# Kernel tuning notes

Hardware: AMD Instinct MI355X
Metric: run time of the kernel (lower is better)

## Reference

```python
import jax, jax.numpy as jnp
import numpy as np
from jax import lax

B, T, H, W, C = 2, 32, 65, 65, 32
KS = 15   # kernel_size
F = 32    # conv features


def setup_inputs() -> dict:
    key = jax.random.key(0)
    ks = jax.random.split(key, 12)
    d = {}
    d["input_seq"] = jax.random.normal(ks[0], (B, T, H, W, C), jnp.float32)
    d["conv_w"] = jax.random.normal(ks[1], (3, 3, C, F), jnp.float32) / np.sqrt(3 * 3 * C).astype(np.float32)
    d["conv_b"] = jnp.zeros((F,), jnp.float32)
    for i, nm in enumerate(["alpha", "delta", "mu", "gamma"]):
        d[f"w_{nm}"] = jax.random.normal(ks[2 + i], (F, C), jnp.float32) / np.sqrt(F).astype(np.float32)
        d[f"b_{nm}"] = jnp.zeros((C,), jnp.float32)
    # nn.initializers.normal() -> stddev 0.01
    d["k_exc"] = jax.random.normal(ks[10], (KS, KS, C), jnp.float32) * 0.01
    d["k_inh"] = jax.random.normal(ks[11], (KS, KS, C), jnp.float32) * 0.01
    return d


def _kernel_spec(k, Hh, Ww):
    # zero-pad the (KS,KS,C) kernel to (H,W,C), then rfft2 over spatial axes
    ph, pw = (Hh - KS) // 2, (Ww - KS) // 2
    kp = jnp.pad(k, ((ph, ph), (pw, pw), (0, 0)))
    return jnp.fft.rfft2(kp, axes=(0, 1))  # (H, W//2+1, C) complex64


def reference(input_seq, conv_w, conv_b, w_alpha, b_alpha, w_delta, b_delta,
              w_mu, b_mu, w_gamma, b_gamma, k_exc, k_inh):
    Bb, Tt, Hh, Ww, Cc = input_seq.shape
    # context conv: flax Conv flattens leading (B,T) into batch; SAME, stride 2
    x = input_seq.reshape(Bb * Tt, Hh, Ww, Cc)
    stats = lax.conv_general_dilated(x, conv_w, (2, 2), 'SAME',
                                     dimension_numbers=('NHWC', 'HWIO', 'NHWC')) + conv_b
    stats = jax.nn.gelu(stats)  # flax nn.gelu (approximate)
    Hp, Wp = stats.shape[1], stats.shape[2]
    stats = stats.reshape(Bb, Tt, Hp, Wp, F)
    ctx = jnp.mean(stats, axis=(1, 2))                 # (B, Wp, F); Wp == W//2+1 for odd W
    alpha = jax.nn.sigmoid(ctx @ w_alpha + b_alpha)    # (B, Wp, C)
    delta = jax.nn.sigmoid(ctx @ w_delta + b_delta)
    mu = jax.nn.softplus(ctx @ w_mu + b_mu)
    gamma = jax.nn.softplus(ctx @ w_gamma + b_gamma)

    K_E = _kernel_spec(k_exc, Hh, Ww)  # (H, Wr, C)
    K_I = _kernel_spec(k_inh, Hh, Ww)
    Wr = Ww // 2 + 1
    decay = jnp.asarray(0.9, jnp.complex64)

    bc = lambda v: jnp.broadcast_to(v[:, None, :, :].astype(jnp.complex64), (Bb, Hh, Wr, Cc))
    A_xx = decay * bc(alpha)
    A_yy = decay * bc(delta)
    A_xy = -K_I[None] * bc(mu)
    A_yx = K_E[None] * bc(gamma)
    row0 = jnp.stack([A_xx, A_xy], axis=-1)
    row1 = jnp.stack([A_yx, A_yy], axis=-1)
    K_hat = jnp.stack([row0, row1], axis=-2)           # (B, H, Wr, C, 2, 2)

    U_hat = jnp.fft.rfft2(input_seq, axes=(2, 3))      # (B, T, H, Wr, C) complex64
    U_vec = jnp.stack([U_hat, jnp.zeros_like(U_hat)], axis=-1)  # (B,T,H,Wr,C,2)
    A_t = jnp.broadcast_to(K_hat[:, None], (Bb, Tt, Hh, Wr, Cc, 2, 2))

    # associative op for linear SSM: state_t = A_t @ state_{t-1} + u_t
    # (log/exp of the original cancel: exp(log A)=A, exp(State_log)=State)
    def combine(l, r):
        A1, b1 = l
        A2, b2 = r
        A = jnp.einsum('...ij,...jk->...ik', A2, A1)
        b = jnp.einsum('...ij,...j->...i', A2, b1) + b2
        return A, b

    _, S = lax.associative_scan(combine, (A_t, U_vec), axis=1)
    Y = S[..., 1]                                      # inhibitory component
    return jnp.fft.irfft2(Y, axes=(2, 3))              # (B, T, H, 2*(Wr-1), C) float32
```

## Files before the change

### kernel.cpp

```cpp
#include <hip/hip_runtime.h>
#include <cmath>

#define NB 2
#define NT 32
#define NH 65
#define NW 65
#define NC 32
#define NF 32
#define NKS 15
#define NHP 33
#define NWP 33
#define NWR 33
#define NWOUT 64
#define PI_F 3.14159265358979323846f

using bf16x8 = __attribute__((ext_vector_type(8))) __bf16;
using f32x4  = __attribute__((ext_vector_type(4))) float;
using s16x4  = __attribute__((ext_vector_type(4))) short;

__device__ inline unsigned short f2bf(float v) {
    unsigned u = __float_as_uint(v);
    u = u + 0x7FFF + ((u >> 16) & 1);
    return (unsigned short)(u >> 16);
}
__device__ inline float bf2f(unsigned short h) {
    return __uint_as_float((unsigned)h << 16);
}

union FragU { s16x4 h[2]; bf16x8 v; };

__global__ __launch_bounds__(256) void setup_kernel(
    const float* __restrict__ w, unsigned short* __restrict__ wBh,
    unsigned short* __restrict__ wBl,
    float2* __restrict__ twr, float2* __restrict__ twb, float2* __restrict__ twi)
{
    int blk = blockIdx.x;
    if (blk < 10) {
        int tid = blk * 256 + threadIdx.x;
        if (tid < NH * 36) {
            int q = tid / 36, wr = tid % 36;
            float2 v = make_float2(0.f, 0.f);
            if (wr < NWR) {
                int p = (q * wr) % NH;
                float a = -2.f * PI_F * (float)p / (float)NH;
                v = make_float2(cosf(a), sinf(a));
            }
            twr[tid] = v;
        }
        if (tid < NH * 14) {
            int h = tid / 14, b = tid % 14;
            float2 v = make_float2(0.f, 0.f);
            if (b < 13) {
                int p = (h * b) % NH;
                float a = 2.f * PI_F * (float)p / (float)NH;
                v = make_float2(cosf(a), sinf(a));
            }
            twb[tid] = v;
        }
        if (tid < 31 * 64) {
            int q = tid / 64 + 1, ow = tid % 64;
            int p = (q * ow) & 63;
            float a = 2.f * PI_F * (float)p / (float)NWOUT;
            twi[tid] = make_float2(cosf(a), sinf(a));
        }
    } else {
        int tid = (blk - 10) * 256 + threadIdx.x;
        if (tid < 9 * NF * NC) {
            int dd = tid / 1024;
            int f = (tid / 32) % 32;
            int c = tid % 32;
            float v = w[((size_t)dd * NC + c) * NF + f];
            unsigned short h = f2bf(v);
            wBh[tid] = h;
            wBl[tid] = f2bf(v - bf2f(h));
        }
    }
}

__global__ __launch_bounds__(256) void conv_mfma_kernel(
    const float* __restrict__ x, const unsigned short* __restrict__ wBh,
    const unsigned short* __restrict__ wBl, const float* __restrict__ bias,
    float* __restrict__ partial)
{
    __shared__ unsigned short aH[3 * 68 * 36];
    __shared__ unsigned short aL[3 * 68 * 36];
    int blk = blockIdx.x;
    int i = blk % NHP;
    int bt = blk / NHP;
    int tid = threadIdx.x;
    int l = tid & 63;
    int w = tid >> 6;

    int nt = w & 1;
    int fcol = nt * 16 + (l & 15);
    int c0 = (l >> 4) * 8;
    bf16x8 bh[9], bl[9];
    #pragma unroll
    for (int dd = 0; dd < 9; ++dd) {
        bh[dd] = *(const bf16x8*)(wBh + dd * 1024 + fcol * 32 + c0);
        bl[dd] = *(const bf16x8*)(wBl + dd * 1024 + fcol * 32 + c0);
    }

    const float* xb = x + (size_t)bt * (NH * NW * NC);
    for (int q = tid; q < 3 * 68 * 8; q += 256) {
        int r = q / 544;
        int k = q % 544;
        int pcol = k >> 3;
        int c4 = (k & 7) * 4;
        int gr = 2 * i - 1 + r;
        int gcol = pcol - 1;
        float4 v = make_float4(0.f, 0.f, 0.f, 0.f);
        if (gr >= 0 && gr < NH && gcol >= 0 && gcol < NW)
            v = *(const float4*)(xb + ((size_t)gr * NW + gcol) * NC + c4);
        int base = (r * 68 + pcol) * 36 + c4;
        unsigned short h0 = f2bf(v.x), h1 = f2bf(v.y), h2 = f2bf(v.z), h3 = f2bf(v.w);
        s16x4 th = {(short)h0, (short)h1, (short)h2, (short)h3};
        *(s16x4*)(aH + base) = th;
        s16x4 tl = {(short)f2bf(v.x - bf2f(h0)), (short)f2bf(v.y - bf2f(h1)),
                    (short)f2bf(v.z - bf2f(h2)), (short)f2bf(v.w - bf2f(h3))};
        *(s16x4*)(aL + base) = tl;
    }
    __syncthreads();

    float bv = bias[fcol];
    f32x4 acc0 = {bv, bv, bv, bv};
    f32x4 acc1 = {bv, bv, bv, bv};
    const int mtA = (w >> 1) ? 1 : 0;
    const bool hasB = (w >> 1) == 0;
    int m15 = l & 15;

    #pragma unroll
    for (int dd = 0; dd < 9; ++dd) {
        const int di = dd / 3, dj = dd % 3;
        {
            int pcol = 2 * (mtA * 16 + m15) + dj;
            int off = (di * 68 + pcol) * 36 + c0;
            FragU ah, al;
            ah.h[0] = *(const s16x4*)(aH + off);
            ah.h[1] = *(const s16x4*)(aH + off + 4);
            al.h[0] = *(const s16x4*)(aL + off);
            al.h[1] = *(const s16x4*)(aL + off + 4);
            acc0 = __builtin_amdgcn_mfma_f32_16x16x32_bf16(al.v, bh[dd], acc0, 0, 0, 0);
            acc0 = __builtin_amdgcn_mfma_f32_16x16x32_bf16(ah.v, bl[dd], acc0, 0, 0, 0);
            acc0 = __builtin_amdgcn_mfma_f32_16x16x32_bf16(ah.v, bh[dd], acc0, 0, 0, 0);
        }
        if (hasB) {
            int pcol = 2 * (32 + m15) + dj;
            if (pcol > 67) pcol = 67;
            int off = (di * 68 + pcol) * 36 + c0;
            FragU ah, al;
            ah.h[0] = *(const s16x4*)(aH + off);
            ah.h[1] = *(const s16x4*)(aH + off + 4);
            al.h[0] = *(const s16x4*)(aL + off);
            al.h[1] = *(const s16x4*)(aL + off + 4);
            acc1 = __builtin_amdgcn_mfma_f32_16x16x32_bf16(al.v, bh[dd], acc1, 0, 0, 0);
            acc1 = __builtin_amdgcn_mfma_f32_16x16x32_bf16(ah.v, bl[dd], acc1, 0, 0, 0);
            acc1 = __builtin_amdgcn_mfma_f32_16x16x32_bf16(ah.v, bh[dd], acc1, 0, 0, 0);
        }
    }

    float* pout = partial + (size_t)blk * (NWP * NF);
    int g4 = (l >> 4) * 4;
    #define GELU(v) (0.5f * (v) * (1.f + tanhf(0.7978845608028654f * ((v) + 0.044715f * (v) * (v) * (v)))))
    #pragma unroll
    for (int r = 0; r < 4; ++r) {
        float v = acc0[r];
        pout[(mtA * 16 + g4 + r) * NF + fcol] = GELU(v);
    }
    if (hasB && g4 == 0) {
        float v = acc1[0];
        pout[32 * NF + fcol] = GELU(v);
    }
    #undef GELU
}

__global__ __launch_bounds__(256) void ctx_reduce1_kernel(
    const float* __restrict__ partial, float* __restrict__ red2)
{
    __shared__ float red[4][64];
    int blk = blockIdx.x;
    int b = blk / 136;
    int rem = blk % 136;
    int chunk = rem / 8;
    int ts = rem % 8;
    int lane = threadIdx.x & 63;
    int tig = threadIdx.x >> 6;
    int jf = chunk * 64 + lane;
    float s0 = 0.f, s1 = 0.f, s2 = 0.f;
    if (jf < NWP * NF) {
        const float* p = partial + (size_t)b * (NT * NHP) * (NWP * NF)
                       + (size_t)(ts * 132 + tig * 33) * (NWP * NF) + jf;
        #pragma unroll 3
        for (int s = 0; s < 33; s += 3) {
            s0 += p[(size_t)s * (NWP * NF)];
            s1 += p[(size_t)(s + 1) * (NWP * NF)];
            s2 += p[(size_t)(s + 2) * (NWP * NF)];
        }
    }
    red[tig][lane] = s0 + s1 + s2;
    __syncthreads();
    if (threadIdx.x < 64) {
        float tot = red[0][threadIdx.x] + red[1][threadIdx.x] +
                    red[2][threadIdx.x] + red[3][threadIdx.x];
        red2[((b * 17 + chunk) * 8 + ts) * 64 + threadIdx.x] = tot;
    }
}

__global__ __launch_bounds__(256) void ctx_reduce2_kernel(
    const float* __restrict__ red2, float* __restrict__ ctx)
{
    __shared__ float red[4][64];
    int b = blockIdx.x / 17, chunk = blockIdx.x % 17;
    int lane = threadIdx.x & 63, tg = threadIdx.x >> 6;
    const float* r2 = red2 + ((size_t)(b * 17 + chunk) * 8) * 64;
    float v = r2[(2 * tg) * 64 + lane] + r2[(2 * tg + 1) * 64 + lane];
    red[tg][lane] = v;
    __syncthreads();
    if (threadIdx.x < 64) {
        int jf = chunk * 64 + threadIdx.x;
        if (jf < NWP * NF) {
            float tot = red[0][threadIdx.x] + red[1][threadIdx.x] +
                        red[2][threadIdx.x] + red[3][threadIdx.x];
            ctx[b * (NWP * NF) + jf] = tot * (1.f / (NT * NHP));
        }
    }
}

__global__ __launch_bounds__(256) void gate_kernel(
    const float* __restrict__ ctx,
    const float* __restrict__ wA, const float* __restrict__ bA,
    const float* __restrict__ wD, const float* __restrict__ bD,
    const float* __restrict__ wM, const float* __restrict__ bM,
    const float* __restrict__ wG, const float* __restrict__ bG,
    float* __restrict__ alpha, float* __restrict__ delta,
    float* __restrict__ mu, float* __restrict__ gamma)
{
    int idx = blockIdx.x * 256 + threadIdx.x;
    if (idx >= NB * NWP * NC) return;
    int c = idx % NC;
    int bw = idx / NC;
    float sA = bA[c], sD = bD[c], sM = bM[c], sG = bG[c];
    #pragma unroll
    for (int f = 0; f < NF; ++f) {
        float v = ctx[bw * NF + f];
        sA = fmaf(v, wA[f * NC + c], sA);
        sD = fmaf(v, wD[f * NC + c], sD);
        sM = fmaf(v, wM[f * NC + c], sM);
        sG = fmaf(v, wG[f * NC + c], sG);
    }
    alpha[idx] = 1.f / (1.f + expf(-sA));
    delta[idx] = 1.f / (1.f + expf(-sD));
    mu[idx]    = fmaxf(sM, 0.f) + log1pf(expf(-fabsf(sM)));
    gamma[idx] = fmaxf(sG, 0.f) + log1pf(expf(-fabsf(sG)));
}

__global__ __launch_bounds__(256) void spec_kernel(
    const float* __restrict__ kexc, const float* __restrict__ kinh,
    float2* __restrict__ KE, float2* __restrict__ KI)
{
    __shared__ float2 tw[NH];
    int tid = threadIdx.x;
    if (tid < NH) {
        float a = -2.f * PI_F * (float)tid / (float)NH;
        tw[tid] = make_float2(cosf(a), sinf(a));
    }
    __syncthreads();
    int idx = blockIdx.x * 256 + tid;
    if (idx >= NH * NWR * NC) return;
    int c = idx % NC;
    int rem = idx / NC;
    int wr = rem % NWR;
    int h = rem / NWR;
    float ker = 0, kei = 0, kir = 0, kii = 0;
    int prow = (25 * (h + wr)) % NH;
    for (int i = 0; i < NKS; ++i) {
        int p = prow;
        for (int j = 0; j < NKS; ++j) {
            float2 e = tw[p];
            float ve = kexc[(i * NKS + j) * NC + c];
            float vi = kinh[(i * NKS + j) * NC + c];
            ker = fmaf(ve, e.x, ker); kei = fmaf(ve, e.y, kei);
            kir = fmaf(vi, e.x, kir); kii = fmaf(vi, e.y, kii);
            p += wr; if (p >= NH) p -= NH;
        }
        prow += h; if (prow >= NH) prow -= NH;
    }
    KE[idx] = make_float2(ker, kei);
    KI[idx] = make_float2(kir, kii);
}

__global__ __launch_bounds__(256) void dft_rows_kernel(
    const float* __restrict__ x, const float2* __restrict__ twr_g,
    float2* __restrict__ U1)
{
    __shared__ __align__(16) float row[4][NW * NC];
    __shared__ __align__(16) float2 twt[NH * 36];
    int tid = threadIdx.x;
    int blk = blockIdx.x;
    int grp = blk % 17;
    int bt = blk / 17;
    int hbase = grp * 4;
    int nrows = NH - hbase; if (nrows > 4) nrows = 4;

    const float* xp = x + ((size_t)bt * NH + hbase) * (NW * NC);
    for (int idx = tid; idx < nrows * NW * NC; idx += 256) ((float*)row)[idx] = xp[idx];
    for (int idx = tid; idx < NH * 36; idx += 256) twt[idx] = twr_g[idx];
    __syncthreads();

    int c = tid & 31;
    int jg = tid >> 5;
    float2 acc[4][4];
    #pragma unroll
    for (int r = 0; r < 4; ++r)
        #pragma unroll
        for (int k = 0; k < 4; ++k) acc[r][k] = make_float2(0.f, 0.f);

    const float2* tp = twt + 4 * jg;
    #pragma unroll 5
    for (int q = 0; q < NW; ++q) {
        float4 e01 = *(const float4*)&tp[q * 36];
        float4 e23 = *(const float4*)&tp[q * 36 + 2];
        #pragma unroll
        for (int r = 0; r < 4; ++r) {
            float v = row[r][q * NC + c];
            acc[r][0].x = fmaf(v, e01.x, acc[r][0].x); acc[r][0].y = fmaf(v, e01.y, acc[r][0].y);
            acc[r][1].x = fmaf(v, e01.z, acc[r][1].x); acc[r][1].y = fmaf(v, e01.w, acc[r][1].y);
            acc[r][2].x = fmaf(v, e23.x, acc[r][2].x); acc[r][2].y = fmaf(v, e23.y, acc[r][2].y);
            acc[r][3].x = fmaf(v, e23.z, acc[r][3].x); acc[r][3].y = fmaf(v, e23.w, acc[r][3].y);
        }
    }
    #pragma unroll
    for (int r = 0; r < 4; ++r) {
        if (r < nrows) {
            float2* up = U1 + ((size_t)bt * NH + hbase + r) * (NWR * NC);
            up[(4 * jg + 0) * NC + c] = acc[r][0];
            up[(4 * jg + 1) * NC + c] = acc[r][1];
            up[(4 * jg + 2) * NC + c] = acc[r][2];
            up[(4 * jg + 3) * NC + c] = acc[r][3];
        }
    }
    if (jg == 0) {
        float2 a32[4];
        #pragma unroll
        for (int r = 0; r < 4; ++r) a32[r] = make_float2(0.f, 0.f);
        #pragma unroll 5
        for (int q = 0; q < NW; ++q) {
            float2 e = twt[q * 36 + 32];
            #pragma unroll
            for (int r = 0; r < 4; ++r) {
                float v = row[r][q * NC + c];
                a32[r].x = fmaf(v, e.x, a32[r].x);
                a32[r].y = fmaf(v, e.y, a32[r].y);
            }
        }
        #pragma unroll
        for (int r = 0; r < 4; ++r)
            if (r < nrows)
                U1[((size_t)bt * NH + hbase + r) * (NWR * NC) + 32 * NC + c] = a32[r];
    }
}

template <int SIGN>
__device__ inline void compute5(const float2 v[5], float2* outp) {
    const float C5[5] = {1.f, 0.30901699437494742f, -0.80901699437494745f,
                         -0.80901699437494745f, 0.30901699437494742f};
    const float S5[5] = {0.f, 0.95105651629515357f, 0.58778525229247314f,
                         -0.58778525229247314f, -0.95105651629515357f};
    #pragma unroll
    for (int r = 0; r < 5; ++r) {
        float re = 0.f, im = 0.f;
        #pragma unroll
        for (int a = 0; a < 5; ++a) {
            const int m = (r * a) % 5;
            const float ex = C5[m];
            const float ey = (float)SIGN * S5[m];
            re = fmaf(v[a].x, ex, fmaf(-v[a].y, ey, re));
            im = fmaf(v[a].x, ey, fmaf(v[a].y, ex, im));
        }
        outp[r * NC] = make_float2(re, im);
    }
}

template <int SIGN, bool SCALE>
__global__ __launch_bounds__(256) void dft_cols_kernel(
    const float2* __restrict__ in, float2* __restrict__ out,
    const float2* __restrict__ twb_g)
{
    __shared__ __align__(16) float2 col[NH * NC];
    __shared__ __align__(16) float2 twb[NH * 14];
    int tid = threadIdx.x;
    int blk = blockIdx.x;
    int wr = blk % NWR;
    int bt = blk / NWR;
    const float2* ip = in + ((size_t)bt * NH) * (NWR * NC) + wr * NC;
    for (int idx = tid; idx < NH * NC; idx += 256) {
        int p = idx >> 5, c = idx & 31;
        col[idx] = ip[(size_t)p * (NWR * NC) + c];
    }
    for (int idx = tid; idx < NH * 14; idx += 256) twb[idx] = twb_g[idx];
    __syncthreads();

    float2 va0[5], va1[5];
    int bq0 = tid >> 5, c0 = tid & 31;
    int q1 = tid + 256;
    int bq1 = q1 >> 5, c1 = q1 & 31;
    #pragma unroll
    for (int a = 0; a < 5; ++a) {
        va0[a] = col[(13 * a + bq0) * NC + c0];
        if (q1 < 416) va1[a] = col[(13 * a + bq1) * NC + c1];
    }
    __syncthreads();
    compute5<SIGN>(va0, &col[(bq0 * 5) * NC + c0]);
    if (q1 < 416) compute5<SIGN>(va1, &col[(bq1 * 5) * NC + c1]);
    __syncthreads();

    const float S = (float)SIGN;
    int c = tid & 31;
    int h0 = tid >> 5;
    const float s = SCALE ? (1.f / (float)NH) : 1.f;
    float2* op = out + ((size_t)bt * NH) * (NWR * NC) + wr * NC;
    float2 acc[8];
    #pragma unroll
    for (int k = 0; k < 8; ++k) {
        int h = h0 + 8 * k;
        int r = h % 5;
        const float2* Ap = col + r * NC + c;
        const float2* tp = twb + h * 14;
        float re = 0.f, im = 0.f;
        #pragma unroll
        for (int p = 0; p < 6; ++p) {
            float4 tq = *(const float4*)&tp[2 * p];
            float2 v0 = Ap[(2 * p) * 5 * NC];
            float2 v1 = Ap[(2 * p + 1) * 5 * NC];
            re = fmaf(v0.x, tq.x, fmaf(-S * v0.y, tq.y, re));
            im = fmaf(S * v0.x, tq.y, fmaf(v0.y, tq.x, im));
            re = fmaf(v1.x, tq.z, fmaf(-S * v1.y, tq.w, re));
            im = fmaf(S * v1.x, tq.w, fmaf(v1.y, tq.z, im));
        }
        {
            float2 t12 = tp[12];
            float2 v = Ap[12 * 5 * NC];
            re = fmaf(v.x, t12.x, fmaf(-S * v.y, t12.y, re));
            im = fmaf(S * v.x, t12.y, fmaf(v.y, t12.x, im));
        }
        acc[k] = make_float2(re * s, im * s);
    }
    #pragma unroll
    for (int k = 0; k < 8; ++k) {
        int h = h0 + 8 * k;
        op[(size_t)h * (NWR * NC) + c] = acc[k];
    }
    if (h0 == 0) {
        const float2* Ap = col + 4 * NC + c;
        const float2* tp = twb + 64 * 14;
        float re = 0.f, im = 0.f;
        #pragma unroll
        for (int p = 0; p < 6; ++p) {
            float4 tq = *(const float4*)&tp[2 * p];
            float2 v0 = Ap[(2 * p) * 5 * NC];
            float2 v1 = Ap[(2 * p + 1) * 5 * NC];
            re = fmaf(v0.x, tq.x, fmaf(-S * v0.y, tq.y, re));
            im = fmaf(S * v0.x, tq.y, fmaf(v0.y, tq.x, im));
            re = fmaf(v1.x, tq.z, fmaf(-S * v1.y, tq.w, re));
            im = fmaf(S * v1.x, tq.w, fmaf(v1.y, tq.z, im));
        }
        {
            float2 t12 = tp[12];
            float2 v = Ap[12 * 5 * NC];
            re = fmaf(v.x, t12.x, fmaf(-S * v.y, t12.y, re));
            im = fmaf(S * v.x, t12.y, fmaf(v.y, t12.x, im));
        }
        op[(size_t)64 * (NWR * NC) + c] = make_float2(re * s, im * s);
    }
}

__global__ __launch_bounds__(256) void scan_kernel(
    float2* __restrict__ buf, const float2* __restrict__ KE,
    const float2* __restrict__ KI, const float* __restrict__ alpha,
    const float* __restrict__ delta, const float* __restrict__ mu,
    const float* __restrict__ gamma)
{
    int idx = blockIdx.x * 256 + threadIdx.x;
    if (idx >= NB * NH * NWR * NC) return;
    int c = idx % NC;
    int rem = idx / NC;
    int wr = rem % NWR;
    int rem2 = rem / NWR;
    int h = rem2 % NH;
    int b = rem2 / NH;

    int gi = (b * NWP + wr) * NC + c;
    float axx = 0.9f * alpha[gi];
    float ayy = 0.9f * delta[gi];
    float m = mu[gi], g = gamma[gi];
    float2 ki = KI[(h * NWR + wr) * NC + c];
    float2 ke = KE[(h * NWR + wr) * NC + c];
    float2 axy = make_float2(-ki.x * m, -ki.y * m);
    float2 ayx = make_float2(ke.x * g, ke.y * g);

    float2 xs = make_float2(0.f, 0.f), ys = make_float2(0.f, 0.f);
    size_t base = ((size_t)b * NT) * NH * NWR * NC + (size_t)h * (NWR * NC) + wr * NC + c;
    const size_t stride = (size_t)NH * NWR * NC;
    for (int t = 0; t < NT; ++t) {
        float2 U = buf[base + (size_t)t * stride];
        float2 nx, ny;
        nx.x = fmaf(axx, xs.x, fmaf(axy.x, ys.x, fmaf(-axy.y, ys.y, U.x)));
        nx.y = fmaf(axx, xs.y, fmaf(axy.x, ys.y, fmaf(axy.y, ys.x, U.y)));
        ny.x = fmaf(ayx.x, xs.x, fmaf(-ayx.y, xs.y, ayy * ys.x));
        ny.y = fmaf(ayx.x, xs.y, fmaf(ayx.y, xs.x, ayy * ys.y));
        xs = nx; ys = ny;
        buf[base + (size_t)t * stride] = ys;
    }
}

__global__ __launch_bounds__(256) void irfft_w_kernel(
    const float2* __restrict__ Z, const float2* __restrict__ twi_g,
    float* __restrict__ out)
{
    __shared__ __align__(16) float2 z[4][NWR * NC];
    __shared__ __align__(16) float2 twi[31 * 64];
    int tid = threadIdx.x;
    int blk = blockIdx.x;
    int grp = blk % 17;
    int bt = blk / 17;
    int hbase = grp * 4;
    int nrows = NH - hbase; if (nrows > 4) nrows = 4;

    const float2* zp = Z + ((size_t)bt * NH + hbase) * (NWR * NC);
    for (int idx = tid; idx < nrows * NWR * NC; idx += 256) ((float2*)z)[idx] = zp[idx];
    for (int idx = tid; idx < 31 * 64; idx += 256) twi[idx] = twi_g[idx];
    __syncthreads();

    int c = tid & 31;
    int g = tid >> 5;
    float acc[4][8];
    #pragma unroll
    for (int r = 0; r < 4; ++r) {
        float z0 = z[r][c].x;
        float zn = z[r][32 * NC + c].x;
        #pragma unroll
        for (int m = 0; m < 8; ++m) acc[r][m] = z0 + ((m & 1) ? -zn : zn);
    }
    const float2* tp = twi + 8 * g;
    for (int q = 1; q < 32; ++q) {
        const float4* tq = (const float4*)&tp[(q - 1) * 64];
        float4 e0 = tq[0], e1 = tq[1], e2 = tq[2], e3 = tq[3];
        #pragma unroll
        for (int r = 0; r < 4; ++r) {
            float2 v = z[r][q * NC + c];
            float vx = 2.f * v.x, vy = 2.f * v.y;
            acc[r][0] = fmaf(vx, e0.x, fmaf(-vy, e0.y, acc[r][0]));
            acc[r][1] = fmaf(vx, e0.z, fmaf(-vy, e0.w, acc[r][1]));
            acc[r][2] = fmaf(vx, e1.x, fmaf(-vy, e1.y, acc[r][2]));
            acc[r][3] = fmaf(vx, e1.z, fmaf(-vy, e1.w, acc[r][3]));
            acc[r][4] = fmaf(vx, e2.x, fmaf(-vy, e2.y, acc[r][4]));
            acc[r][5] = fmaf(vx, e2.z, fmaf(-vy, e2.w, acc[r][5]));
            acc[r][6] = fmaf(vx, e3.x, fmaf(-vy, e3.y, acc[r][6]));
            acc[r][7] = fmaf(vx, e3.z, fmaf(-vy, e3.w, acc[r][7]));
        }
    }
    #pragma unroll
    for (int r = 0; r < 4; ++r) {
        if (r < nrows) {
            float* op = out + ((size_t)bt * NH + hbase + r) * (NWOUT * NC);
            #pragma unroll
            for (int m = 0; m < 8; ++m)
                op[(8 * g + m) * NC + c] = acc[r][m] * (1.f / (float)NWOUT);
        }
    }
}

extern "C" void kernel_launch(void* const* d_in, const int* in_sizes, int n_in,
                              void* d_out, int out_size, void* d_ws, size_t ws_size,
                              hipStream_t stream)
{
    const float* x     = (const float*)d_in[0];
    const float* convw = (const float*)d_in[1];
    const float* convb = (const float*)d_in[2];
    const float* wA = (const float*)d_in[3];
    const float* bA = (const float*)d_in[4];
    const float* wD = (const float*)d_in[5];
    const float* bD = (const float*)d_in[6];
    const float* wM = (const float*)d_in[7];
    const float* bM = (const float*)d_in[8];
    const float* wG = (const float*)d_in[9];
    const float* bG = (const float*)d_in[10];
    const float* kexc = (const float*)d_in[11];
    const float* kinh = (const float*)d_in[12];

    const size_t NBIG = (size_t)NB * NT * NH * NWR * NC;
    char* ws = (char*)d_ws;
    float2* bufA    = (float2*)ws;  ws += NBIG * sizeof(float2);
    float2* KE      = (float2*)ws;  ws += (size_t)NH * NWR * NC * sizeof(float2);
    float2* KI      = (float2*)ws;  ws += (size_t)NH * NWR * NC * sizeof(float2);
    float*  partial = (float*)ws;   ws += (size_t)NB * (NT * NHP) * (NWP * NF) * sizeof(float);
    float*  ctx     = (float*)ws;   ws += (size_t)NB * NWP * NF * sizeof(float);
    float*  red2    = (float*)ws;   ws += (size_t)NB * 17 * 8 * 64 * sizeof(float);
    float*  alpha   = (float*)ws;   ws += (size_t)NB * NWP * NC * sizeof(float);
    float*  delta   = (float*)ws;   ws += (size_t)NB * NWP * NC * sizeof(float);
    float*  mu      = (float*)ws;   ws += (size_t)NB * NWP * NC * sizeof(float);
    float*  gamma   = (float*)ws;   ws += (size_t)NB * NWP * NC * sizeof(float);
    float2* TWR     = (float2*)ws;  ws += (size_t)NH * 36 * sizeof(float2);
    float2* TWB     = (float2*)ws;  ws += (size_t)NH * 14 * sizeof(float2);
    float2* TWI     = (float2*)ws;  ws += (size_t)31 * 64 * sizeof(float2);
    unsigned short* wBh = (unsigned short*)ws; ws += (size_t)9 * NC * NF * sizeof(unsigned short);
    unsigned short* wBl = (unsigned short*)ws; ws += (size_t)9 * NC * NF * sizeof(unsigned short);

    setup_kernel<<<46, 256, 0, stream>>>(convw, wBh, wBl, TWR, TWB, TWI);

    conv_mfma_kernel<<<NB * NT * NHP, 256, 0, stream>>>(x, wBh, wBl, convb, partial);
    ctx_reduce1_kernel<<<NB * 136, 256, 0, stream>>>(partial, red2);
    ctx_reduce2_kernel<<<NB * 17, 256, 0, stream>>>(red2, ctx);
    gate_kernel<<<(NB * NWP * NC + 255) / 256, 256, 0, stream>>>(
        ctx, wA, bA, wD, bD, wM, bM, wG, bG, alpha, delta, mu, gamma);

    spec_kernel<<<(NH * NWR * NC + 255) / 256, 256, 0, stream>>>(kexc, kinh, KE, KI);

    dft_rows_kernel<<<NB * NT * 17, 256, 0, stream>>>(x, TWR, bufA);
    dft_cols_kernel<-1, false><<<NB * NT * NWR, 256, 0, stream>>>(bufA, bufA, TWB);

    scan_kernel<<<(NB * NH * NWR * NC + 255) / 256, 256, 0, stream>>>(
        bufA, KE, KI, alpha, delta, mu, gamma);

    dft_cols_kernel<+1, true><<<NB * NT * NWR, 256, 0, stream>>>(bufA, bufA, TWB);
    irfft_w_kernel<<<NB * NT * 17, 256, 0, stream>>>(bufA, TWI, (float*)d_out);
}
```

Before: 175.6 us.

## Fuse column DFT, temporal scan, and inverse column DFT into one kernel

Replaces the forward column DFT, the SSM scan, and the inverse column DFT kernels with a single kernel. Each block owns one (batch, wr, 16-channel half) slice, loops over time, and keeps the scan state in registers while doing both column transforms in shared memory. This removes two full round trips of the spectral buffer through global memory and two launches. In exchange the grid shrinks to 132 blocks, each running a serial time loop with four barriers per step, so occupancy and parallelism drop sharply.

Result: slower. 254.1 us (+44.7%).

```diff
diff --git a/kernel.cpp b/kernel.cpp
--- a/kernel.cpp
+++ b/kernel.cpp
@@ -361,7 +361,7 @@
 }
 
 template <int SIGN>
-__device__ inline void compute5(const float2 v[5], float2* outp) {
+__device__ inline void compute5s(const float2 v[5], float2* outp) {
     const float C5[5] = {1.f, 0.30901699437494742f, -0.80901699437494745f,
                          -0.80901699437494745f, 0.30901699437494742f};
     const float S5[5] = {0.f, 0.95105651629515357f, 0.58778525229247314f,
@@ -377,139 +377,113 @@
             re = fmaf(v[a].x, ex, fmaf(-v[a].y, ey, re));
             im = fmaf(v[a].x, ey, fmaf(v[a].y, ex, im));
         }
-        outp[r * NC] = make_float2(re, im);
-    }
-}
-
-template <int SIGN, bool SCALE>
-__global__ __launch_bounds__(256) void dft_cols_kernel(
-    const float2* __restrict__ in, float2* __restrict__ out,
-    const float2* __restrict__ twb_g)
-{
-    __shared__ __align__(16) float2 col[NH * NC];
+        outp[r * 17] = make_float2(re, im);
+    }
+}
+
+__global__ __launch_bounds__(256) void ssm_spectral_kernel(
+    float2* __restrict__ buf, const float2* __restrict__ twb_g,
+    const float2* __restrict__ KE, const float2* __restrict__ KI,
+    const float* __restrict__ alpha, const float* __restrict__ delta,
+    const float* __restrict__ mu, const float* __restrict__ gamma)
+{
+    __shared__ __align__(16) float2 lin[NH * 17];
+    __shared__ __align__(16) float2 lA[NH * 17];
     __shared__ __align__(16) float2 twb[NH * 14];
     int tid = threadIdx.x;
     int blk = blockIdx.x;
-    int wr = blk % NWR;
-    int bt = blk / NWR;
-    const float2* ip = in + ((size_t)bt * NH) * (NWR * NC) + wr * NC;
-    for (int idx = tid; idx < NH * NC; idx += 256) {
-        int p = idx >> 5, c = idx & 31;
-        col[idx] = ip[(size_t)p * (NWR * NC) + c];
-    }
+    int ch = blk & 1;
+    int wr = (blk >> 1) % NWR;
+    int b  = blk / (2 * NWR);
+    int cc = tid & 15;
+    int hg = tid >> 4;
+    int cg = ch * 16 + cc;
+
     for (int idx = tid; idx < NH * 14; idx += 256) twb[idx] = twb_g[idx];
-    __syncthreads();
-
-    float2 va0[5], va1[5];
-    int bq0 = tid >> 5, c0 = tid & 31;
-    int q1 = tid + 256;
-    int bq1 = q1 >> 5, c1 = q1 & 31;
-    #pragma unroll
-    for (int a = 0; a < 5; ++a) {
-        va0[a] = col[(13 * a + bq0) * NC + c0];
-        if (q1 < 416) va1[a] = col[(13 * a + bq1) * NC + c1];
-    }
-    __syncthreads();
-    compute5<SIGN>(va0, &col[(bq0 * 5) * NC + c0]);
-    if (q1 < 416) compute5<SIGN>(va1, &col[(bq1 * 5) * NC + c1]);
-    __syncthreads();
-
-    const float S = (float)SIGN;
-    int c = tid & 31;
-    int h0 = tid >> 5;
-    const float s = SCALE ? (1.f / (float)NH) : 1.f;
-    float2* op = out + ((size_t)bt * NH) * (NWR * NC) + wr * NC;
-    float2 acc[8];
-    #pragma unroll
-    for (int k = 0; k < 8; ++k) {
-        int h = h0 + 8 * k;
-        int r = h % 5;
-        const float2* Ap = col + r * NC + c;
-        const float2* tp = twb + h * 14;
-        float re = 0.f, im = 0.f;
-        #pragma unroll
-        for (int p = 0; p < 6; ++p) {
-            float4 tq = *(const float4*)&tp[2 * p];
-            float2 v0 = Ap[(2 * p) * 5 * NC];
-            float2 v1 = Ap[(2 * p + 1) * 5 * NC];
-            re = fmaf(v0.x, tq.x, fmaf(-S * v0.y, tq.y, re));
-            im = fmaf(S * v0.x, tq.y, fmaf(v0.y, tq.x, im));
-            re = fmaf(v1.x, tq.z, fmaf(-S * v1.y, tq.w, re));
-            im = fmaf(S * v1.x, tq.w, fmaf(v1.y, tq.z, im));
-        }
-        {
-            float2 t12 = tp[12];
-            float2 v = Ap[12 * 5 * NC];
-            re = fmaf(v.x, t12.x, fmaf(-S * v.y, t12.y, re));
-            im = fmaf(S * v.x, t12.y, fmaf(v.y, t12.x, im));
-        }
-        acc[k] = make_float2(re * s, im * s);
-    }
-    #pragma unroll
-    for (int k = 0; k < 8; ++k) {
-        int h = h0 + 8 * k;
-        op[(size_t)h * (NWR * NC) + c] = acc[k];
-    }
-    if (h0 == 0) {
-        const float2* Ap = col + 4 * NC + c;
-        const float2* tp = twb + 64 * 14;
-        float re = 0.f, im = 0.f;
-        #pragma unroll
-        for (int p = 0; p < 6; ++p) {
-            float4 tq = *(const float4*)&tp[2 * p];
-            float2 v0 = Ap[(2 * p) * 5 * NC];
-            float2 v1 = Ap[(2 * p + 1) * 5 * NC];
-            re = fmaf(v0.x, tq.x, fmaf(-S * v0.y, tq.y, re));
-            im = fmaf(S * v0.x, tq.y, fmaf(v0.y, tq.x, im));
-            re = fmaf(v1.x, tq.z, fmaf(-S * v1.y, tq.w, re));
-            im = fmaf(S * v1.x, tq.w, fmaf(v1.y, tq.z, im));
-        }
-        {
-            float2 t12 = tp[12];
-            float2 v = Ap[12 * 5 * NC];
-            re = fmaf(v.x, t12.x, fmaf(-S * v.y, t12.y, re));
-            im = fmaf(S * v.x, t12.y, fmaf(v.y, t12.x, im));
-        }
-        op[(size_t)64 * (NWR * NC) + c] = make_float2(re * s, im * s);
-    }
-}
-
-__global__ __launch_bounds__(256) void scan_kernel(
-    float2* __restrict__ buf, const float2* __restrict__ KE,
-    const float2* __restrict__ KI, const float* __restrict__ alpha,
-    const float* __restrict__ delta, const float* __restrict__ mu,
-    const float* __restrict__ gamma)
-{
-    int idx = blockIdx.x * 256 + threadIdx.x;
-    if (idx >= NB * NH * NWR * NC) return;
-    int c = idx % NC;
-    int rem = idx / NC;
-    int wr = rem % NWR;
-    int rem2 = rem / NWR;
-    int h = rem2 % NH;
-    int b = rem2 / NH;
-
-    int gi = (b * NWP + wr) * NC + c;
-    float axx = 0.9f * alpha[gi];
-    float ayy = 0.9f * delta[gi];
+
+    int gi = (b * NWP + wr) * NC + cg;
+    float axx = 0.9f * alpha[gi], ayy = 0.9f * delta[gi];
     float m = mu[gi], g = gamma[gi];
-    float2 ki = KI[(h * NWR + wr) * NC + c];
-    float2 ke = KE[(h * NWR + wr) * NC + c];
-    float2 axy = make_float2(-ki.x * m, -ki.y * m);
-    float2 ayx = make_float2(ke.x * g, ke.y * g);
-
-    float2 xs = make_float2(0.f, 0.f), ys = make_float2(0.f, 0.f);
-    size_t base = ((size_t)b * NT) * NH * NWR * NC + (size_t)h * (NWR * NC) + wr * NC + c;
-    const size_t stride = (size_t)NH * NWR * NC;
+    float2 axy[5], ayx[5], xs[5], ys[5];
+    int hv[5], rof[5], tof[5];
+    bool val[5];
+    #pragma unroll
+    for (int k = 0; k < 5; ++k) {
+        int h = hg + 16 * k;
+        val[k] = (h < NH);
+        int hh = val[k] ? h : 0;
+        hv[k] = hh;
+        rof[k] = (hh % 5) * 17 + cc;
+        tof[k] = hh * 14;
+        float2 ki = KI[((size_t)hh * NWR + wr) * NC + cg];
+        float2 ke = KE[((size_t)hh * NWR + wr) * NC + cg];
+        axy[k] = make_float2(-ki.x * m, -ki.y * m);
+        ayx[k] = make_float2(ke.x * g, ke.y * g);
+        xs[k] = make_float2(0.f, 0.f);
+        ys[k] = make_float2(0.f, 0.f);
+    }
+    const size_t tstride = (size_t)NH * NWR * NC;
+    float2* base = buf + (size_t)(b * NT) * tstride + (size_t)wr * NC + ch * 16;
+
     for (int t = 0; t < NT; ++t) {
-        float2 U = buf[base + (size_t)t * stride];
-        float2 nx, ny;
-        nx.x = fmaf(axx, xs.x, fmaf(axy.x, ys.x, fmaf(-axy.y, ys.y, U.x)));
-        nx.y = fmaf(axx, xs.y, fmaf(axy.x, ys.y, fmaf(axy.y, ys.x, U.y)));
-        ny.x = fmaf(ayx.x, xs.x, fmaf(-ayx.y, xs.y, ayy * ys.x));
-        ny.y = fmaf(ayx.x, xs.y, fmaf(ayx.y, xs.x, ayy * ys.y));
-        xs = nx; ys = ny;
-        buf[base + (size_t)t * stride] = ys;
+        float2* bt = base + (size_t)t * tstride;
+        for (int idx = tid; idx < NH * 16; idx += 256) {
+            int h = idx >> 4, c = idx & 15;
+            lin[h * 17 + c] = bt[(size_t)h * (NWR * NC) + c];
+        }
+        __syncthreads();
+        if (hg < 13) {
+            float2 va[5];
+            #pragma unroll
+            for (int a = 0; a < 5; ++a) va[a] = lin[(13 * a + hg) * 17 + cc];
+            compute5s<-1>(va, &lA[(hg * 5) * 17 + cc]);
+        }
+        __syncthreads();
+        #pragma unroll
+        for (int k = 0; k < 5; ++k) {
+            if (!val[k]) continue;
+            const float2* Ap = lA + rof[k];
+            const float2* tp = twb + tof[k];
+            float re = 0.f, im = 0.f;
+            #pragma unroll
+            for (int bq = 0; bq < 13; ++bq) {
+                float2 e = tp[bq];
+                float2 v = Ap[bq * 85];
+                re = fmaf(v.x, e.x, fmaf(v.y, e.y, re));
+                im = fmaf(-v.x, e.y, fmaf(v.y, e.x, im));
+            }
+            float2 nx, ny;
+            nx.x = fmaf(axx, xs[k].x, fmaf(axy[k].x, ys[k].x, fmaf(-axy[k].y, ys[k].y, re)));
+            nx.y = fmaf(axx, xs[k].y, fmaf(axy[k].x, ys[k].y, fmaf(axy[k].y, ys[k].x, im)));
+            ny.x = fmaf(ayx[k].x, xs[k].x, fmaf(-ayx[k].y, xs[k].y, ayy * ys[k].x));
+            ny.y = fmaf(ayx[k].x, xs[k].y, fmaf(ayx[k].y, xs[k].x, ayy * ys[k].y));
+            xs[k] = nx; ys[k] = ny;
+            lin[hv[k] * 17 + cc] = ny;
+        }
+        __syncthreads();
+        if (hg < 13) {
+            float2 va[5];
+            #pragma unroll
+            for (int a = 0; a < 5; ++a) va[a] = lin[(13 * a + hg) * 17 + cc];
+            compute5s<+1>(va, &lA[(hg * 5) * 17 + cc]);
+        }
+        __syncthreads();
+        #pragma unroll
+        for (int k = 0; k < 5; ++k) {
+            if (!val[k]) continue;
+            const float2* Ap = lA + rof[k];
+            const float2* tp = twb + tof[k];
+            float re = 0.f, im = 0.f;
+            #pragma unroll
+            for (int bq = 0; bq < 13; ++bq) {
+                float2 e = tp[bq];
+                float2 v = Ap[bq * 85];
+                re = fmaf(v.x, e.x, fmaf(-v.y, e.y, re));
+                im = fmaf(v.x, e.y, fmaf(v.y, e.x, im));
+            }
+            bt[(size_t)hv[k] * (NWR * NC) + cc] =
+                make_float2(re * (1.f / NH), im * (1.f / NH));
+        }
     }
 }
 
@@ -617,11 +591,9 @@
     spec_kernel<<<(NH * NWR * NC + 255) / 256, 256, 0, stream>>>(kexc, kinh, KE, KI);
 
     dft_rows_kernel<<<NB * NT * 17, 256, 0, stream>>>(x, TWR, bufA);
-    dft_cols_kernel<-1, false><<<NB * NT * NWR, 256, 0, stream>>>(bufA, bufA, TWB);
-
-    scan_kernel<<<(NB * NH * NWR * NC + 255) / 256, 256, 0, stream>>>(
-        bufA, KE, KI, alpha, delta, mu, gamma);
-
-    dft_cols_kernel<+1, true><<<NB * NT * NWR, 256, 0, stream>>>(bufA, bufA, TWB);
+
+    ssm_spectral_kernel<<<NB * NWR * 2, 256, 0, stream>>>(
+        bufA, TWB, KE, KI, alpha, delta, mu, gamma);
+
     irfft_w_kernel<<<NB * NT * 17, 256, 0, stream>>>(bufA, TWI, (float*)d_out);
 }
```

## Fuse spec into setup, merge ctx reduce with gates, batch two columns per DFT block

Applied to the files above, without the earlier changes.

The kernel-spectrum computation moves into extra blocks of the setup kernel, and the second ctx reduction is fused with the gate projection. Both changes cut the launch count by two. The column DFT kernels now handle two wr columns per block with a doubled shared buffer, which halves the grid and amortizes the twiddle load. The cost is more shared memory and registers per block in the column DFT, which may lower occupancy.

New measurement: 254.5 us. +44.9%, slower.

```diff
diff --git a/kernel.cpp b/kernel.cpp
--- a/kernel.cpp
+++ b/kernel.cpp
@@ -32,7 +32,9 @@
 __global__ __launch_bounds__(256) void setup_kernel(
     const float* __restrict__ w, unsigned short* __restrict__ wBh,
     unsigned short* __restrict__ wBl,
-    float2* __restrict__ twr, float2* __restrict__ twb, float2* __restrict__ twi)
+    float2* __restrict__ twr, float2* __restrict__ twb, float2* __restrict__ twi,
+    const float* __restrict__ kexc, const float* __restrict__ kinh,
+    float2* __restrict__ KE, float2* __restrict__ KI)
 {
     int blk = blockIdx.x;
     if (blk < 10) {
@@ -63,7 +65,7 @@
             float a = 2.f * PI_F * (float)p / (float)NWOUT;
             twi[tid] = make_float2(cosf(a), sinf(a));
         }
-    } else {
+    } else if (blk < 46) {
         int tid = (blk - 10) * 256 + threadIdx.x;
         if (tid < 9 * NF * NC) {
             int dd = tid / 1024;
@@ -74,6 +76,36 @@
             wBh[tid] = h;
             wBl[tid] = f2bf(v - bf2f(h));
         }
+    } else {
+        __shared__ float2 tw[NH];
+        int tid = threadIdx.x;
+        if (tid < NH) {
+            float a = -2.f * PI_F * (float)tid / (float)NH;
+            tw[tid] = make_float2(cosf(a), sinf(a));
+        }
+        __syncthreads();
+        int idx = (blk - 46) * 256 + tid;
+        if (idx >= NH * NWR * NC) return;
+        int c = idx % NC;
+        int rem = idx / NC;
+        int wr = rem % NWR;
+        int h = rem / NWR;
+        float ker = 0, kei = 0, kir = 0, kii = 0;
+        int prow = (25 * (h + wr)) % NH;
+        for (int i = 0; i < NKS; ++i) {
+            int p = prow;
+            for (int j = 0; j < NKS; ++j) {
+                float2 e = tw[p];
+                float ve = kexc[(i * NKS + j) * NC + c];
+                float vi = kinh[(i * NKS + j) * NC + c];
+                ker = fmaf(ve, e.x, ker); kei = fmaf(ve, e.y, kei);
+                kir = fmaf(vi, e.x, kir); kii = fmaf(vi, e.y, kii);
+                p += wr; if (p >= NH) p -= NH;
+            }
+            prow += h; if (prow >= NH) prow -= NH;
+        }
+        KE[idx] = make_float2(ker, kei);
+        KI[idx] = make_float2(kir, kii);
     }
 }
 
@@ -206,28 +238,8 @@
     }
 }
 
-__global__ __launch_bounds__(256) void ctx_reduce2_kernel(
-    const float* __restrict__ red2, float* __restrict__ ctx)
-{
-    __shared__ float red[4][64];
-    int b = blockIdx.x / 17, chunk = blockIdx.x % 17;
-    int lane = threadIdx.x & 63, tg = threadIdx.x >> 6;
-    const float* r2 = red2 + ((size_t)(b * 17 + chunk) * 8) * 64;
-    float v = r2[(2 * tg) * 64 + lane] + r2[(2 * tg + 1) * 64 + lane];
-    red[tg][lane] = v;
-    __syncthreads();
-    if (threadIdx.x < 64) {
-        int jf = chunk * 64 + threadIdx.x;
-        if (jf < NWP * NF) {
-            float tot = red[0][threadIdx.x] + red[1][threadIdx.x] +
-                        red[2][threadIdx.x] + red[3][threadIdx.x];
-            ctx[b * (NWP * NF) + jf] = tot * (1.f / (NT * NHP));
-        }
-    }
-}
-
-__global__ __launch_bounds__(256) void gate_kernel(
-    const float* __restrict__ ctx,
+__global__ __launch_bounds__(256) void ctx2_gate_kernel(
+    const float* __restrict__ red2,
     const float* __restrict__ wA, const float* __restrict__ bA,
     const float* __restrict__ wD, const float* __restrict__ bD,
     const float* __restrict__ wM, const float* __restrict__ bM,
@@ -235,58 +247,41 @@
     float* __restrict__ alpha, float* __restrict__ delta,
     float* __restrict__ mu, float* __restrict__ gamma)
 {
-    int idx = blockIdx.x * 256 + threadIdx.x;
-    if (idx >= NB * NWP * NC) return;
-    int c = idx % NC;
-    int bw = idx / NC;
-    float sA = bA[c], sD = bD[c], sM = bM[c], sG = bG[c];
-    #pragma unroll
-    for (int f = 0; f < NF; ++f) {
-        float v = ctx[bw * NF + f];
-        sA = fmaf(v, wA[f * NC + c], sA);
-        sD = fmaf(v, wD[f * NC + c], sD);
-        sM = fmaf(v, wM[f * NC + c], sM);
-        sG = fmaf(v, wG[f * NC + c], sG);
-    }
-    alpha[idx] = 1.f / (1.f + expf(-sA));
-    delta[idx] = 1.f / (1.f + expf(-sD));
-    mu[idx]    = fmaxf(sM, 0.f) + log1pf(expf(-fabsf(sM)));
-    gamma[idx] = fmaxf(sG, 0.f) + log1pf(expf(-fabsf(sG)));
-}
-
-__global__ __launch_bounds__(256) void spec_kernel(
-    const float* __restrict__ kexc, const float* __restrict__ kinh,
-    float2* __restrict__ KE, float2* __restrict__ KI)
-{
-    __shared__ float2 tw[NH];
-    int tid = threadIdx.x;
-    if (tid < NH) {
-        float a = -2.f * PI_F * (float)tid / (float)NH;
-        tw[tid] = make_float2(cosf(a), sinf(a));
-    }
-    __syncthreads();
-    int idx = blockIdx.x * 256 + tid;
-    if (idx >= NH * NWR * NC) return;
-    int c = idx % NC;
-    int rem = idx / NC;
-    int wr = rem % NWR;
-    int h = rem / NWR;
-    float ker = 0, kei = 0, kir = 0, kii = 0;
-    int prow = (25 * (h + wr)) % NH;
-    for (int i = 0; i < NKS; ++i) {
-        int p = prow;
-        for (int j = 0; j < NKS; ++j) {
-            float2 e = tw[p];
-            float ve = kexc[(i * NKS + j) * NC + c];
-            float vi = kinh[(i * NKS + j) * NC + c];
-            ker = fmaf(ve, e.x, ker); kei = fmaf(ve, e.y, kei);
-            kir = fmaf(vi, e.x, kir); kii = fmaf(vi, e.y, kii);
-            p += wr; if (p >= NH) p -= NH;
-        }
-        prow += h; if (prow >= NH) prow -= NH;
-    }
-    KE[idx] = make_float2(ker, kei);
-    KI[idx] = make_float2(kir, kii);
+    __shared__ float red[4][64];
+    __shared__ float ctxs[64];
+    int b = blockIdx.x / 17, chunk = blockIdx.x % 17;
+    int lane = threadIdx.x & 63, tg = threadIdx.x >> 6;
+    const float* r2 = red2 + ((size_t)(b * 17 + chunk) * 8) * 64;
+    float v = r2[(2 * tg) * 64 + lane] + r2[(2 * tg + 1) * 64 + lane];
+    red[tg][lane] = v;
+    __syncthreads();
+    if (threadIdx.x < 64) {
+        int jf = chunk * 64 + threadIdx.x;
+        float tot = 0.f;
+        if (jf < NWP * NF)
+            tot = (red[0][threadIdx.x] + red[1][threadIdx.x] +
+                   red[2][threadIdx.x] + red[3][threadIdx.x]) * (1.f / (NT * NHP));
+        ctxs[threadIdx.x] = tot;
+    }
+    __syncthreads();
+
+    int g = threadIdx.x >> 6;
+    int jl = (threadIdx.x >> 5) & 1;
+    int c = threadIdx.x & 31;
+    int j = chunk * 2 + jl;
+    if (j < NWP) {
+        const float* W  = (g == 0) ? wA : (g == 1) ? wD : (g == 2) ? wM : wG;
+        const float* Bv = (g == 0) ? bA : (g == 1) ? bD : (g == 2) ? bM : bG;
+        float s = Bv[c];
+        #pragma unroll
+        for (int f = 0; f < NF; ++f)
+            s = fmaf(ctxs[jl * 32 + f], W[f * NC + c], s);
+        float r;
+        if (g < 2) r = 1.f / (1.f + expf(-s));
+        else       r = fmaxf(s, 0.f) + log1pf(expf(-fabsf(s)));
+        float* outp = (g == 0) ? alpha : (g == 1) ? delta : (g == 2) ? mu : gamma;
+        outp[(b * NWP + j) * NC + c] = r;
+    }
 }
 
 __global__ __launch_bounds__(256) void dft_rows_kernel(
@@ -316,6 +311,7 @@
         for (int k = 0; k < 4; ++k) acc[r][k] = make_float2(0.f, 0.f);
 
     const float2* tp = twt + 4 * jg;
+    const int nr = nrows;
     #pragma unroll 5
     for (int q = 0; q < NW; ++q) {
         float4 e01 = *(const float4*)&tp[q * 36];
@@ -331,7 +327,7 @@
     }
     #pragma unroll
     for (int r = 0; r < 4; ++r) {
-        if (r < nrows) {
+        if (r < nr) {
             float2* up = U1 + ((size_t)bt * NH + hbase + r) * (NWR * NC);
             up[(4 * jg + 0) * NC + c] = acc[r][0];
             up[(4 * jg + 1) * NC + c] = acc[r][1];
@@ -355,7 +351,7 @@
         }
         #pragma unroll
         for (int r = 0; r < 4; ++r)
-            if (r < nrows)
+            if (r < nr)
                 U1[((size_t)bt * NH + hbase + r) * (NWR * NC) + 32 * NC + c] = a32[r];
     }
 }
@@ -386,91 +382,107 @@
     const float2* __restrict__ in, float2* __restrict__ out,
     const float2* __restrict__ twb_g)
 {
-    __shared__ __align__(16) float2 col[NH * NC];
+    __shared__ __align__(16) float2 col[2][NH * NC];
     __shared__ __align__(16) float2 twb[NH * 14];
     int tid = threadIdx.x;
     int blk = blockIdx.x;
-    int wr = blk % NWR;
-    int bt = blk / NWR;
-    const float2* ip = in + ((size_t)bt * NH) * (NWR * NC) + wr * NC;
-    for (int idx = tid; idx < NH * NC; idx += 256) {
-        int p = idx >> 5, c = idx & 31;
-        col[idx] = ip[(size_t)p * (NWR * NC) + c];
+    int wrp = blk % 17;
+    int bt = blk / 17;
+    int wr0 = 2 * wrp;
+    int nwr = NWR - wr0; if (nwr > 2) nwr = 2;
+
+    const float2* ip = in + ((size_t)bt * NH) * (NWR * NC) + wr0 * NC;
+    for (int idx = tid; idx < nwr * NH * NC; idx += 256) {
+        int wl = idx / (NH * NC);
+        int rest = idx % (NH * NC);
+        int p = rest >> 5, c = rest & 31;
+        col[wl][rest] = ip[(size_t)p * (NWR * NC) + wl * NC + c];
     }
     for (int idx = tid; idx < NH * 14; idx += 256) twb[idx] = twb_g[idx];
     __syncthreads();
 
-    float2 va0[5], va1[5];
-    int bq0 = tid >> 5, c0 = tid & 31;
-    int q1 = tid + 256;
-    int bq1 = q1 >> 5, c1 = q1 & 31;
-    #pragma unroll
-    for (int a = 0; a < 5; ++a) {
-        va0[a] = col[(13 * a + bq0) * NC + c0];
-        if (q1 < 416) va1[a] = col[(13 * a + bq1) * NC + c1];
-    }
-    __syncthreads();
-    compute5<SIGN>(va0, &col[(bq0 * 5) * NC + c0]);
-    if (q1 < 416) compute5<SIGN>(va1, &col[(bq1 * 5) * NC + c1]);
+    float2 va[4][5];
+    int ubq[4], uc[4], uw[4];
+    bool uval[4];
+    #pragma unroll
+    for (int s = 0; s < 4; ++s) {
+        int q = tid + 256 * s;
+        uval[s] = (q < nwr * 416);
+        int qq = uval[s] ? q : 0;
+        uw[s] = qq / 416;
+        int r2 = qq % 416;
+        ubq[s] = r2 >> 5;
+        uc[s] = r2 & 31;
+        #pragma unroll
+        for (int a = 0; a < 5; ++a)
+            va[s][a] = col[uw[s]][(13 * a + ubq[s]) * NC + uc[s]];
+    }
+    __syncthreads();
+    #pragma unroll
+    for (int s = 0; s < 4; ++s)
+        if (uval[s])
+            compute5<SIGN>(va[s], &col[uw[s]][(ubq[s] * 5) * NC + uc[s]]);
     __syncthreads();
 
     const float S = (float)SIGN;
     int c = tid & 31;
     int h0 = tid >> 5;
     const float s = SCALE ? (1.f / (float)NH) : 1.f;
-    float2* op = out + ((size_t)bt * NH) * (NWR * NC) + wr * NC;
-    float2 acc[8];
-    #pragma unroll
-    for (int k = 0; k < 8; ++k) {
-        int h = h0 + 8 * k;
-        int r = h % 5;
-        const float2* Ap = col + r * NC + c;
-        const float2* tp = twb + h * 14;
-        float re = 0.f, im = 0.f;
-        #pragma unroll
-        for (int p = 0; p < 6; ++p) {
-            float4 tq = *(const float4*)&tp[2 * p];
-            float2 v0 = Ap[(2 * p) * 5 * NC];
-            float2 v1 = Ap[(2 * p + 1) * 5 * NC];
-            re = fmaf(v0.x, tq.x, fmaf(-S * v0.y, tq.y, re));
-            im = fmaf(S * v0.x, tq.y, fmaf(v0.y, tq.x, im));
-            re = fmaf(v1.x, tq.z, fmaf(-S * v1.y, tq.w, re));
-            im = fmaf(S * v1.x, tq.w, fmaf(v1.y, tq.z, im));
-        }
-        {
-            float2 t12 = tp[12];
-            float2 v = Ap[12 * 5 * NC];
-            re = fmaf(v.x, t12.x, fmaf(-S * v.y, t12.y, re));
-            im = fmaf(S * v.x, t12.y, fmaf(v.y, t12.x, im));
-        }
-        acc[k] = make_float2(re * s, im * s);
-    }
-    #pragma unroll
-    for (int k = 0; k < 8; ++k) {
-        int h = h0 + 8 * k;
-        op[(size_t)h * (NWR * NC) + c] = acc[k];
-    }
-    if (h0 == 0) {
-        const float2* Ap = col + 4 * NC + c;
-        const float2* tp = twb + 64 * 14;
-        float re = 0.f, im = 0.f;
-        #pragma unroll
-        for (int p = 0; p < 6; ++p) {
-            float4 tq = *(const float4*)&tp[2 * p];
-            float2 v0 = Ap[(2 * p) * 5 * NC];
-            float2 v1 = Ap[(2 * p + 1) * 5 * NC];
-            re = fmaf(v0.x, tq.x, fmaf(-S * v0.y, tq.y, re));
-            im = fmaf(S * v0.x, tq.y, fmaf(v0.y, tq.x, im));
-            re = fmaf(v1.x, tq.z, fmaf(-S * v1.y, tq.w, re));
-            im = fmaf(S * v1.x, tq.w, fmaf(v1.y, tq.z, im));
-        }
-        {
-            float2 t12 = tp[12];
-            float2 v = Ap[12 * 5 * NC];
-            re = fmaf(v.x, t12.x, fmaf(-S * v.y, t12.y, re));
-            im = fmaf(S * v.x, t12.y, fmaf(v.y, t12.x, im));
-        }
-        op[(size_t)64 * (NWR * NC) + c] = make_float2(re * s, im * s);
+    for (int wl = 0; wl < nwr; ++wl) {
+        float2* op = out + ((size_t)bt * NH) * (NWR * NC) + (wr0 + wl) * NC;
+        float2 acc[8];
+        #pragma unroll
+        for (int k = 0; k < 8; ++k) {
+            int h = h0 + 8 * k;
+            int r = h % 5;
+            const float2* Ap = col[wl] + r * NC + c;
+            const float2* tp = twb + h * 14;
+            float re = 0.f, im = 0.f;
+            #pragma unroll
+            for (int p = 0; p < 6; ++p) {
+                float4 tq = *(const float4*)&tp[2 * p];
+                float2 v0 = Ap[(2 * p) * 5 * NC];
+                float2 v1 = Ap[(2 * p + 1) * 5 * NC];
+                re = fmaf(v0.x, tq.x, fmaf(-S * v0.y, tq.y, re));
+                im = fmaf(S * v0.x, tq.y, fmaf(v0.y, tq.x, im));
+                re = fmaf(v1.x, tq.z, fmaf(-S * v1.y, tq.w, re));
+                im = fmaf(S * v1.x, tq.w, fmaf(v1.y, tq.z, im));
+            }
+            {
+                float2 t12 = tp[12];
+                float2 v = Ap[12 * 5 * NC];
+                re = fmaf(v.x, t12.x, fmaf(-S * v.y, t12.y, re));
+                im = fmaf(S * v.x, t12.y, fmaf(v.y, t12.x, im));
+            }
+            acc[k] = make_float2(re * s, im * s);
+        }
+        #pragma unroll
+        for (int k = 0; k < 8; ++k) {
+            int h = h0 + 8 * k;
+            op[(size_t)h * (NWR * NC) + c] = acc[k];
+        }
+        if (h0 == 0) {
+            const float2* Ap = col[wl] + 4 * NC + c;
+            const float2* tp = twb + 64 * 14;
+            float re = 0.f, im = 0.f;
+            #pragma unroll
+            for (int p = 0; p < 6; ++p) {
+                float4 tq = *(const float4*)&tp[2 * p];
+                float2 v0 = Ap[(2 * p) * 5 * NC];
+                float2 v1 = Ap[(2 * p + 1) * 5 * NC];
+                re = fmaf(v0.x, tq.x, fmaf(-S * v0.y, tq.y, re));
+                im = fmaf(S * v0.x, tq.y, fmaf(v0.y, tq.x, im));
+                re = fmaf(v1.x, tq.z, fmaf(-S * v1.y, tq.w, re));
+                im = fmaf(S * v1.x, tq.w, fmaf(v1.y, tq.z, im));
+            }
+            {
+                float2 t12 = tp[12];
+                float2 v = Ap[12 * 5 * NC];
+                re = fmaf(v.x, t12.x, fmaf(-S * v.y, t12.y, re));
+                im = fmaf(S * v.x, t12.y, fmaf(v.y, t12.x, im));
+            }
+            op[(size_t)64 * (NWR * NC) + c] = make_float2(re * s, im * s);
+        }
     }
 }
 
@@ -594,7 +606,6 @@
     float2* KE      = (float2*)ws;  ws += (size_t)NH * NWR * NC * sizeof(float2);
     float2* KI      = (float2*)ws;  ws += (size_t)NH * NWR * NC * sizeof(float2);
     float*  partial = (float*)ws;   ws += (size_t)NB * (NT * NHP) * (NWP * NF) * sizeof(float);
-    float*  ctx     = (float*)ws;   ws += (size_t)NB * NWP * NF * sizeof(float);
     float*  red2    = (float*)ws;   ws += (size_t)NB * 17 * 8 * 64 * sizeof(float);
     float*  alpha   = (float*)ws;   ws += (size_t)NB * NWP * NC * sizeof(float);
     float*  delta   = (float*)ws;   ws += (size_t)NB * NWP * NC * sizeof(float);
@@ -606,22 +617,20 @@
     unsigned short* wBh = (unsigned short*)ws; ws += (size_t)9 * NC * NF * sizeof(unsigned short);
     unsigned short* wBl = (unsigned short*)ws; ws += (size_t)9 * NC * NF * sizeof(unsigned short);
 
-    setup_kernel<<<46, 256, 0, stream>>>(convw, wBh, wBl, TWR, TWB, TWI);
+    setup_kernel<<<46 + 268, 256, 0, stream>>>(convw, wBh, wBl, TWR, TWB, TWI,
+                                               kexc, kinh, KE, KI);
 
     conv_mfma_kernel<<<NB * NT * NHP, 256, 0, stream>>>(x, wBh, wBl, convb, partial);
     ctx_reduce1_kernel<<<NB * 136, 256, 0, stream>>>(partial, red2);
-    ctx_reduce2_kernel<<<NB * 17, 256, 0, stream>>>(red2, ctx);
-    gate_kernel<<<(NB * NWP * NC + 255) / 256, 256, 0, stream>>>(
-        ctx, wA, bA, wD, bD, wM, bM, wG, bG, alpha, delta, mu, gamma);
-
-    spec_kernel<<<(NH * NWR * NC + 255) / 256, 256, 0, stream>>>(kexc, kinh, KE, KI);
+    ctx2_gate_kernel<<<NB * 17, 256, 0, stream>>>(
+        red2, wA, bA, wD, bD, wM, bM, wG, bG, alpha, delta, mu, gamma);
 
     dft_rows_kernel<<<NB * NT * 17, 256, 0, stream>>>(x, TWR, bufA);
-    dft_cols_kernel<-1, false><<<NB * NT * NWR, 256, 0, stream>>>(bufA, bufA, TWB);
+    dft_cols_kernel<-1, false><<<NB * NT * 17, 256, 0, stream>>>(bufA, bufA, TWB);
 
     scan_kernel<<<(NB * NH * NWR * NC + 255) / 256, 256, 0, stream>>>(
         bufA, KE, KI, alpha, delta, mu, gamma);
 
-    dft_cols_kernel<+1, true><<<NB * NT * NWR, 256, 0, stream>>>(bufA, bufA, TWB);
+    dft_cols_kernel<+1, true><<<NB * NT * 17, 256, 0, stream>>>(bufA, bufA, TWB);
     irfft_w_kernel<<<NB * NT * 17, 256, 0, stream>>>(bufA, TWI, (float*)d_out);
 }
```
